# Optimization experiments

Measured on AMD Instinct MI355X. Metric: run time of the kernel, lower is better.

## Reference

```python
import jax, jax.numpy as jnp
import numpy as np

D_MODEL, NUM_HEADS, D_HEAD, N_CTX = 768, 12, 64, 2048
BATCH = 2


def setup_inputs() -> dict:
    key = jax.random.key(0)
    kx, kk, kq, kv, ko = jax.random.split(key, 5)
    s = 1.0 / np.sqrt(D_MODEL).astype(np.float32)
    x = jax.random.normal(kx, (BATCH, N_CTX, D_MODEL), dtype=jnp.float32)
    W_K = jax.random.normal(kk, (NUM_HEADS, D_HEAD, D_MODEL), dtype=jnp.float32) * s
    W_Q = jax.random.normal(kq, (NUM_HEADS, D_HEAD, D_MODEL), dtype=jnp.float32) * s
    W_V = jax.random.normal(kv, (NUM_HEADS, D_HEAD, D_MODEL), dtype=jnp.float32) * s
    W_O = jax.random.normal(ko, (D_MODEL, D_HEAD * NUM_HEADS), dtype=jnp.float32) * s
    return {"x": x, "W_K": W_K, "W_Q": W_Q, "W_V": W_V, "W_O": W_O}


def reference(x, W_K, W_Q, W_V, W_O):
    B, P, _ = x.shape
    d_head = W_K.shape[1]
    # per-head projections: [B, H, P, d_head]
    q = jnp.einsum('hed,bpd->bhpe', W_Q, x)
    k = jnp.einsum('hed,bpd->bhpe', W_K, x)
    v = jnp.einsum('hed,bpd->bhpe', W_V, x)
    # causal scores [B, H, Q, K]
    scores = jnp.einsum('bhqe,bhke->bhqk', q, k) / np.sqrt(d_head).astype(np.float32)
    mask = jnp.tril(jnp.ones((P, P), dtype=bool))
    scores = jnp.where(mask, scores, jnp.asarray(-1e9, scores.dtype))
    attn = jax.nn.softmax(scores, axis=-1)
    z = jnp.einsum('bhqk,bhke->bhqe', attn, v)
    # flatten heads head-major: 'b h q e -> b q (h e)'
    z_flat = z.transpose(0, 2, 1, 3).reshape(B, P, -1)
    return jnp.einsum('bpf,df->bpd', z_flat, W_O)
```

## Files before the change

kernel.cpp:

```cpp
#include <hip/hip_runtime.h>
#include <hip/hip_bf16.h>

typedef __attribute__((ext_vector_type(8))) short bf16x8;
typedef __attribute__((ext_vector_type(4))) float f32x4;
typedef __attribute__((ext_vector_type(16))) float f32x16;

static __device__ __forceinline__ unsigned short f2bf(float f) {
  union { float f; unsigned int u; } v; v.f = f;
  unsigned int u = v.u;
  return (unsigned short)((u + 0x7FFFu + ((u >> 16) & 1u)) >> 16);
}

__device__ __forceinline__ void async_ld16(const void* g, void* l) {
  __builtin_amdgcn_global_load_lds(
      (const __attribute__((address_space(1))) unsigned int*)g,
      (__attribute__((address_space(3))) unsigned int*)l, 16, 0, 0);
}

__global__ __launch_bounds__(256) void cvt_all(
    const float* __restrict__ x, const float* __restrict__ wk,
    const float* __restrict__ wq, const float* __restrict__ wv,
    const float* __restrict__ wo,
    unsigned short* __restrict__ x_bf, unsigned short* __restrict__ wkqv4,
    unsigned short* __restrict__ wo4) {
  int i = blockIdx.x * 256 + threadIdx.x;
  int e0 = i * 4;
  if (e0 < 3145728) {
    float4 v = *(const float4*)(x + e0);
    ushort4 r;
    r.x = f2bf(v.x); r.y = f2bf(v.y); r.z = f2bf(v.z); r.w = f2bf(v.w);
    *(ushort4*)(x_bf + e0) = r;
    return;
  }
  int j = e0 - 3145728;
  int a = j / 589824;
  int off = j - a * 589824;
  int nl = off / 768;
  int k = off - nl * 768;
  const float* src;
  unsigned short* dst;
  int m;
  float scale = 1.0f;
  if (a == 0)      { src = wk; m = nl;        dst = wkqv4; }
  else if (a == 1) { src = wq; m = 768 + nl;  dst = wkqv4; scale = 0.18033688011112042f; }
  else if (a == 2) { src = wv; m = 1536 + nl; dst = wkqv4; }
  else             { src = wo; m = nl;        dst = wo4; }
  float4 v = *(const float4*)(src + off);
  long idx = ((long)(m >> 4) * 24 + (k >> 5)) * 512 + (m & 15) * 32 + (k & 31);
  ushort4 r;
  r.x = f2bf(v.x * scale); r.y = f2bf(v.y * scale);
  r.z = f2bf(v.z * scale); r.w = f2bf(v.w * scale);
  *(ushort4*)(dst + idx) = r;
}

template <int MODE>
__device__ __forceinline__ void gemm_body(
    const unsigned short* __restrict__ A,
    const unsigned short* __restrict__ B4,
    void* __restrict__ outK, void* __restrict__ outQ, void* __restrict__ outV,
    int m0, int n0,
    unsigned short (*As)[8192]) {
  const int tid = threadIdx.x;
  const int w = tid >> 6;
  const int l = tid & 63;
  const int g = l >> 4;
  const int c = l & 15;
  const int wr = w >> 1, wc = w & 1;

  f32x4 acc[4][3];
#pragma unroll
  for (int i = 0; i < 4; i++)
#pragma unroll
    for (int j = 0; j < 3; j++) acc[i][j] = (f32x4){0.f, 0.f, 0.f, 0.f};

  const int lrow = l >> 3;
  const int lcolx = ((l & 7) ^ lrow) * 8;
  const unsigned short* pB = B4 + (long)((n0 >> 4) + wc * 3) * 12288 + c * 32 + g * 8;

  auto stageA = [&](int buf, int kt) {
    const int k0 = kt * 64;
#pragma unroll
    for (int cc = 0; cc < 4; ++cc) {
      int chunk = cc * 4 + w;
      int row = chunk * 8 + lrow;
      async_ld16(A + (long)(m0 + row) * 768 + k0 + lcolx, &As[buf][chunk * 512]);
    }
  };

  stageA(0, 0);
  for (int kt = 0; kt < 12; ++kt) {
    const int cur = kt & 1;
    bf16x8 b[2][3];
#pragma unroll
    for (int ks = 0; ks < 2; ++ks)
#pragma unroll
      for (int ni = 0; ni < 3; ++ni)
        b[ks][ni] = *(const bf16x8*)(pB + (long)ni * 12288 + (kt * 2 + ks) * 512);
    __builtin_amdgcn_sched_barrier(0);
    if (kt < 11) {
      stageA(cur ^ 1, kt + 1);
      asm volatile("s_waitcnt vmcnt(4)" ::: "memory");
    } else {
      asm volatile("s_waitcnt vmcnt(0)" ::: "memory");
    }
    __builtin_amdgcn_sched_barrier(0);
    __builtin_amdgcn_s_barrier();
    __builtin_amdgcn_sched_barrier(0);

#pragma unroll
    for (int ks = 0; ks < 2; ++ks) {
      bf16x8 a[4];
#pragma unroll
      for (int mi = 0; mi < 4; ++mi) {
        int row = wr * 64 + mi * 16 + c;
        int col = (ks * 32 + g * 8) ^ ((row & 7) * 8);
        a[mi] = *(const bf16x8*)&As[cur][row * 64 + col];
      }
#pragma unroll
      for (int mi = 0; mi < 4; ++mi)
#pragma unroll
        for (int ni = 0; ni < 3; ++ni)
          acc[mi][ni] = __builtin_amdgcn_mfma_f32_16x16x32_bf16(a[mi], b[ks][ni], acc[mi][ni], 0, 0, 0);
    }
    __builtin_amdgcn_sched_barrier(0);
    asm volatile("s_waitcnt lgkmcnt(0)" ::: "memory");
    __builtin_amdgcn_s_barrier();
    __builtin_amdgcn_sched_barrier(0);
  }

  if (MODE == 1) {
    float* O = (float*)outK;
#pragma unroll
    for (int mi = 0; mi < 4; ++mi)
#pragma unroll
      for (int ni = 0; ni < 3; ++ni)
#pragma unroll
        for (int r = 0; r < 4; ++r) {
          int m = m0 + wr * 64 + mi * 16 + g * 4 + r;
          int n = n0 + wc * 48 + ni * 16 + c;
          O[(long)m * 768 + n] = acc[mi][ni][r];
        }
  } else {
    const int which = (n0 >= 1536) ? 2 : (n0 >= 768 ? 1 : 0);
    const int nb = n0 - which * 768;
#pragma unroll
    for (int mi = 0; mi < 4; ++mi)
#pragma unroll
      for (int ni = 0; ni < 3; ++ni)
#pragma unroll
        for (int r = 0; r < 4; ++r) {
          int m = m0 + wr * 64 + mi * 16 + g * 4 + r;
          int nn = nb + wc * 48 + ni * 16 + c;
          int b = m >> 11, p = m & 2047;
          int h = nn >> 6, e = nn & 63;
          unsigned short val = f2bf(acc[mi][ni][r]);
          long bh = b * 12 + h;
          if (which == 0) {
            long idx = bh * 131072 + (p >> 5) * 2048 + (e >> 4) * 512 + (p & 31) * 16 + (e & 15);
            ((unsigned short*)outK)[idx] = val;
          } else if (which == 1) {
            ((unsigned short*)outQ)[((bh * 2048 + p) << 6) + e] = val;
          } else {
            long idx = bh * 131072 + (p >> 4) * 1024 + e * 16 + (p & 15);
            ((unsigned short*)outV)[idx] = val;
          }
        }
  }
}

__global__ __launch_bounds__(256) void gemm_qkv(
    const unsigned short* __restrict__ A,
    const unsigned short* __restrict__ Wkqv4,
    unsigned short* __restrict__ k4b, unsigned short* __restrict__ qb,
    unsigned short* __restrict__ v4b) {
  __shared__ __align__(16) unsigned short As[2][8192];
  const int lb = blockIdx.x;
  const int xcd = lb & 7, idx = lb >> 3;
  const int mg = xcd >> 1, ng = xcd & 1;
  const int mi = idx / 12, ni = idx - 12 * mi;
  gemm_body<0>(A, Wkqv4, k4b, qb, v4b, (mg * 8 + mi) * 128, (ng * 12 + ni) * 96, As);
}

__global__ __launch_bounds__(256) void gemm_out(
    const unsigned short* __restrict__ A,
    const unsigned short* __restrict__ Wo4,
    float* __restrict__ out) {
  __shared__ __align__(16) unsigned short As[2][8192];
  const int lb = blockIdx.x;
  const int xcd = lb & 7, idx = lb >> 3;
  const int mi = idx >> 3, ni = idx & 7;
  gemm_body<1>(A, Wo4, out, nullptr, nullptr, (xcd * 4 + mi) * 128, ni * 96, As);
}

__global__ __launch_bounds__(256) void attn(
    const unsigned short* __restrict__ Q,
    const unsigned short* __restrict__ K4,
    const unsigned short* __restrict__ V4,
    unsigned short* __restrict__ Z) {
  __shared__ float2 Opart[3][16][64];
  __shared__ float Lpart[3][32];
  __shared__ float Linv[32];
  const int bx = blockIdx.x;
  const int cidx = bx / 24;
  const int bh = bx - cidx * 24;
  const int c = 63 - cidx;
  const int tid = threadIdx.x;
  const int w = tid >> 6;
  const int l = tid & 63;
  const int ql = l & 31;
  const int hi = l >> 5;
  const int b = bh / 12, hd = bh - b * 12;
  const long base = (long)bh * 2048 * 64;
  const int q0 = c * 32;

  bf16x8 qf[4];
  {
    const unsigned short* qp = Q + base + (long)(q0 + ql) * 64 + hi * 8;
#pragma unroll
    for (int d = 0; d < 4; ++d) qf[d] = *(const bf16x8*)(qp + d * 16);
  }

  f32x16 o0, o1;
#pragma unroll
  for (int r = 0; r < 16; ++r) { o0[r] = 0.f; o1[r] = 0.f; }
  float lsum = 0.f;

  const unsigned short* kp = K4 + (long)bh * 131072 + ql * 16 + hi * 8;
  const unsigned short* vp = V4 + (long)bh * 131072 + ql * 16 + hi * 8;

  auto loadsub = [&](bf16x8* kf, bf16x8* v0, bf16x8* v1, int s) {
    const unsigned short* kps = kp + (long)s * 2048;
#pragma unroll
    for (int d = 0; d < 4; ++d) kf[d] = *(const bf16x8*)(kps + d * 512);
    const unsigned short* vps = vp + (long)s * 2048;
    v0[0] = *(const bf16x8*)(vps);
    v0[1] = *(const bf16x8*)(vps + 1024);
    v1[0] = *(const bf16x8*)(vps + 512);
    v1[1] = *(const bf16x8*)(vps + 1536);
  };

  auto compute = [&](const bf16x8* kf, const bf16x8* v0, const bf16x8* v1, bool diag) {
    __builtin_amdgcn_s_setprio(1);
    f32x16 s_;
#pragma unroll
    for (int r = 0; r < 16; ++r) s_[r] = 0.f;
#pragma unroll
    for (int d = 0; d < 4; ++d)
      s_ = __builtin_amdgcn_mfma_f32_32x32x16_bf16(kf[d], qf[d], s_, 0, 0, 0);
    __builtin_amdgcn_s_setprio(0);
    if (diag) {
#pragma unroll
      for (int r = 0; r < 16; ++r) {
        int krow = (r & 3) + 8 * (r >> 2) + 4 * hi;
        s_[r] = (krow <= ql) ? s_[r] : -1e30f;
      }
    }
    float p[16];
#pragma unroll
    for (int r = 0; r < 16; ++r) { p[r] = exp2f(s_[r]); lsum += p[r]; }
    unsigned int wpk[8];
#pragma unroll
    for (int i = 0; i < 8; ++i)
      asm("v_cvt_pk_bf16_f32 %0, %1, %2" : "=v"(wpk[i]) : "v"(p[2 * i]), "v"(p[2 * i + 1]));
    asm volatile("v_permlane32_swap_b32 %0, %1" : "+v"(wpk[0]), "+v"(wpk[2]));
    asm volatile("v_permlane32_swap_b32 %0, %1" : "+v"(wpk[1]), "+v"(wpk[3]));
    asm volatile("v_permlane32_swap_b32 %0, %1" : "+v"(wpk[4]), "+v"(wpk[6]));
    asm volatile("v_permlane32_swap_b32 %0, %1" : "+v"(wpk[5]), "+v"(wpk[7]));
    union { unsigned int u[4]; bf16x8 v; } f0, f1;
    f0.u[0] = wpk[0]; f0.u[1] = wpk[1]; f0.u[2] = wpk[2]; f0.u[3] = wpk[3];
    f1.u[0] = wpk[4]; f1.u[1] = wpk[5]; f1.u[2] = wpk[6]; f1.u[3] = wpk[7];
    __builtin_amdgcn_s_setprio(1);
    o0 = __builtin_amdgcn_mfma_f32_32x32x16_bf16(f0.v, v0[0], o0, 0, 0, 0);
    o1 = __builtin_amdgcn_mfma_f32_32x32x16_bf16(f0.v, v1[0], o1, 0, 0, 0);
    o0 = __builtin_amdgcn_mfma_f32_32x32x16_bf16(f1.v, v0[1], o0, 0, 0, 0);
    o1 = __builtin_amdgcn_mfma_f32_32x32x16_bf16(f1.v, v1[1], o1, 0, 0, 0);
    __builtin_amdgcn_s_setprio(0);
  };

  int s = w;
  if (s <= c) {
    bf16x8 kfA[4], vA0[2], vA1[2], kfB[4], vB0[2], vB1[2];
    loadsub(kfA, vA0, vA1, s);
    while (s + 8 <= c) {
      loadsub(kfB, vB0, vB1, s + 4);
      compute(kfA, vA0, vA1, false);
      loadsub(kfA, vA0, vA1, s + 8);
      compute(kfB, vB0, vB1, false);
      s += 8;
    }
    if (s + 4 <= c) {
      loadsub(kfB, vB0, vB1, s + 4);
      compute(kfA, vA0, vA1, false);
      compute(kfB, vB0, vB1, (s + 4) == c);
    } else {
      compute(kfA, vA0, vA1, s == c);
    }
  }

  lsum += __shfl_xor(lsum, 32);

  if (w) {
#pragma unroll
    for (int r = 0; r < 16; ++r) Opart[w - 1][r][l] = make_float2(o0[r], o1[r]);
    if (l < 32) Lpart[w - 1][l] = lsum;
  }
  __syncthreads();
  if (w == 0) {
    float ltot = lsum + Lpart[0][ql] + Lpart[1][ql] + Lpart[2][ql];
    if (l < 32) Linv[l] = 1.0f / ltot;
#pragma unroll
    for (int r = 0; r < 16; ++r) {
      float2 t0 = Opart[0][r][l], t1 = Opart[1][r][l], t2 = Opart[2][r][l];
      o0[r] += t0.x + t1.x + t2.x;
      o1[r] += t0.y + t1.y + t2.y;
    }
#pragma unroll
    for (int r = 0; r < 16; ++r) {
      int qr = (r & 3) + 8 * (r >> 2) + 4 * hi;
      float li = Linv[qr];
      unsigned short* zp = Z + ((long)(b * 2048 + q0 + qr) * 768 + hd * 64 + ql);
      zp[0]  = f2bf(o0[r] * li);
      zp[32] = f2bf(o1[r] * li);
    }
  }
}

extern "C" void kernel_launch(void* const* d_in, const int* in_sizes, int n_in,
                              void* d_out, int out_size, void* d_ws, size_t ws_size,
                              hipStream_t stream) {
  const float* x  = (const float*)d_in[0];
  const float* wk = (const float*)d_in[1];
  const float* wq = (const float*)d_in[2];
  const float* wv = (const float*)d_in[3];
  const float* wo = (const float*)d_in[4];

  unsigned short* ws = (unsigned short*)d_ws;
  unsigned short* x_bf  = ws;
  unsigned short* wkqv4 = x_bf + 3145728;
  unsigned short* wo4   = wkqv4 + 1769472;
  unsigned short* qb    = wo4 + 589824;
  unsigned short* k4b   = qb + 3145728;
  unsigned short* v4b   = k4b + 3145728;
  unsigned short* zb    = v4b + 3145728;

  cvt_all<<<5376, 256, 0, stream>>>(x, wk, wq, wv, wo, x_bf, wkqv4, wo4);
  gemm_qkv<<<768, 256, 0, stream>>>(x_bf, wkqv4, k4b, qb, v4b);
  attn<<<1536, 256, 0, stream>>>(qb, k4b, v4b, zb);
  gemm_out<<<256, 256, 0, stream>>>(zb, wo4, (float*)d_out);
}
```

Measured before the change: 89.71 us.

## Double-buffer B registers in projection GEMM and vectorize V-output stores

```diff
diff --git a/kernel.cpp b/kernel.cpp
--- a/kernel.cpp
+++ b/kernel.cpp
@@ -86,27 +86,29 @@
       async_ld16(A + (long)(m0 + row) * 768 + k0 + lcolx, &As[buf][chunk * 512]);
     }
   };
-
-  stageA(0, 0);
-  for (int kt = 0; kt < 12; ++kt) {
-    const int cur = kt & 1;
-    bf16x8 b[2][3];
+  auto loadB = [&](bf16x8 (*b)[3], int kt) {
 #pragma unroll
     for (int ks = 0; ks < 2; ++ks)
 #pragma unroll
       for (int ni = 0; ni < 3; ++ni)
         b[ks][ni] = *(const bf16x8*)(pB + (long)ni * 12288 + (kt * 2 + ks) * 512);
-    __builtin_amdgcn_sched_barrier(0);
-    if (kt < 11) {
-      stageA(cur ^ 1, kt + 1);
-      asm volatile("s_waitcnt vmcnt(4)" ::: "memory");
-    } else {
-      asm volatile("s_waitcnt vmcnt(0)" ::: "memory");
-    }
+  };
+  auto step = [&](const bf16x8* asrc, const bf16x8 (*b)[3]) {
+  };
+
+  bf16x8 b0[2][3], b1[2][3];
+  stageA(0, 0);
+  loadB(b0, 0);
+
+#pragma unroll
+  for (int kt = 0; kt < 12; kt += 2) {
+    if (kt + 1 < 12) loadB(b1, kt + 1);
+    __builtin_amdgcn_sched_barrier(0);
+    asm volatile("s_waitcnt vmcnt(6)" ::: "memory");
     __builtin_amdgcn_sched_barrier(0);
     __builtin_amdgcn_s_barrier();
     __builtin_amdgcn_sched_barrier(0);
-
+    if (kt + 1 < 12) stageA(1, kt + 1);
 #pragma unroll
     for (int ks = 0; ks < 2; ++ks) {
       bf16x8 a[4];
@@ -114,18 +116,40 @@
       for (int mi = 0; mi < 4; ++mi) {
         int row = wr * 64 + mi * 16 + c;
         int col = (ks * 32 + g * 8) ^ ((row & 7) * 8);
-        a[mi] = *(const bf16x8*)&As[cur][row * 64 + col];
+        a[mi] = *(const bf16x8*)&As[0][row * 64 + col];
       }
 #pragma unroll
       for (int mi = 0; mi < 4; ++mi)
 #pragma unroll
         for (int ni = 0; ni < 3; ++ni)
-          acc[mi][ni] = __builtin_amdgcn_mfma_f32_16x16x32_bf16(a[mi], b[ks][ni], acc[mi][ni], 0, 0, 0);
-    }
-    __builtin_amdgcn_sched_barrier(0);
-    asm volatile("s_waitcnt lgkmcnt(0)" ::: "memory");
+          acc[mi][ni] = __builtin_amdgcn_mfma_f32_16x16x32_bf16(a[mi], b0[ks][ni], acc[mi][ni], 0, 0, 0);
+    }
+    if (kt + 2 < 12) loadB(b0, kt + 2);
+    __builtin_amdgcn_sched_barrier(0);
+    if (kt + 2 < 12) {
+      asm volatile("s_waitcnt vmcnt(6)" ::: "memory");
+    } else {
+      asm volatile("s_waitcnt vmcnt(0)" ::: "memory");
+    }
+    __builtin_amdgcn_sched_barrier(0);
     __builtin_amdgcn_s_barrier();
     __builtin_amdgcn_sched_barrier(0);
+    if (kt + 2 < 12) stageA(0, kt + 2);
+#pragma unroll
+    for (int ks = 0; ks < 2; ++ks) {
+      bf16x8 a[4];
+#pragma unroll
+      for (int mi = 0; mi < 4; ++mi) {
+        int row = wr * 64 + mi * 16 + c;
+        int col = (ks * 32 + g * 8) ^ ((row & 7) * 8);
+        a[mi] = *(const bf16x8*)&As[1][row * 64 + col];
+      }
+#pragma unroll
+      for (int mi = 0; mi < 4; ++mi)
+#pragma unroll
+        for (int ni = 0; ni < 3; ++ni)
+          acc[mi][ni] = __builtin_amdgcn_mfma_f32_16x16x32_bf16(a[mi], b1[ks][ni], acc[mi][ni], 0, 0, 0);
+    }
   }
 
   if (MODE == 1) {
@@ -143,28 +167,43 @@
   } else {
     const int which = (n0 >= 1536) ? 2 : (n0 >= 768 ? 1 : 0);
     const int nb = n0 - which * 768;
-#pragma unroll
-    for (int mi = 0; mi < 4; ++mi)
-#pragma unroll
-      for (int ni = 0; ni < 3; ++ni)
-#pragma unroll
-        for (int r = 0; r < 4; ++r) {
-          int m = m0 + wr * 64 + mi * 16 + g * 4 + r;
-          int nn = nb + wc * 48 + ni * 16 + c;
-          int b = m >> 11, p = m & 2047;
-          int h = nn >> 6, e = nn & 63;
-          unsigned short val = f2bf(acc[mi][ni][r]);
+    const int b = m0 >> 11;
+    if (which == 2) {
+#pragma unroll
+      for (int mi = 0; mi < 4; ++mi)
+#pragma unroll
+        for (int ni = 0; ni < 3; ++ni) {
+          int e = nb + wc * 48 + ni * 16 + c;
+          int h = e >> 6, el = e & 63;
           long bh = b * 12 + h;
-          if (which == 0) {
-            long idx = bh * 131072 + (p >> 5) * 2048 + (e >> 4) * 512 + (p & 31) * 16 + (e & 15);
-            ((unsigned short*)outK)[idx] = val;
-          } else if (which == 1) {
-            ((unsigned short*)outQ)[((bh * 2048 + p) << 6) + e] = val;
-          } else {
-            long idx = bh * 131072 + (p >> 4) * 1024 + e * 16 + (p & 15);
-            ((unsigned short*)outV)[idx] = val;
+          int p0 = (m0 & 2047) + wr * 64 + mi * 16 + g * 4;
+          long idx = bh * 131072 + (p0 >> 4) * 1024 + el * 16 + (p0 & 15);
+          ushort4 pk;
+          pk.x = f2bf(acc[mi][ni][0]); pk.y = f2bf(acc[mi][ni][1]);
+          pk.z = f2bf(acc[mi][ni][2]); pk.w = f2bf(acc[mi][ni][3]);
+          *(ushort4*)&((unsigned short*)outV)[idx] = pk;
+        }
+    } else {
+#pragma unroll
+      for (int mi = 0; mi < 4; ++mi)
+#pragma unroll
+        for (int ni = 0; ni < 3; ++ni)
+#pragma unroll
+          for (int r = 0; r < 4; ++r) {
+            int m = m0 + wr * 64 + mi * 16 + g * 4 + r;
+            int nn = nb + wc * 48 + ni * 16 + c;
+            int p = m & 2047;
+            int h = nn >> 6, e = nn & 63;
+            unsigned short val = f2bf(acc[mi][ni][r]);
+            long bh = b * 12 + h;
+            if (which == 0) {
+              long idx = bh * 131072 + (p >> 5) * 2048 + (e >> 4) * 512 + (p & 31) * 16 + (e & 15);
+              ((unsigned short*)outK)[idx] = val;
+            } else {
+              ((unsigned short*)outQ)[((bh * 2048 + p) << 6) + e] = val;
+            }
           }
-        }
+    }
   }
 }
 
```

After: 79.36 us. -11.5%, faster.
